# Kernel tuning notes

Hardware: AMD Instinct MI355X
Metric: run time of the kernel (lower is better)

## Reference

```python
import jax, jax.numpy as jnp
import numpy as np

B, L, D_MODEL = 2, 2048, 1024
HEADS, DH, K = 8, 128, 64  # d_head = d_model // heads, kernel_width window
DILATIONS = np.array([1, 1, 2, 2, 4, 4, 8, 8], dtype=np.int32)  # per-head dilation


def setup_inputs() -> dict:
    key = jax.random.key(0)
    ks = jax.random.split(key, 8)
    s_in = 1.0 / np.sqrt(D_MODEL)       # kaiming-uniform-ish fan_in bound
    s_c = 1.0 / np.sqrt(HEADS * DH)
    return {
        "query": jax.random.normal(ks[0], (B, L, D_MODEL), dtype=jnp.float32),
        "key": jax.random.normal(ks[1], (B, L, D_MODEL), dtype=jnp.float32),
        "value": jax.random.normal(ks[2], (B, L, D_MODEL), dtype=jnp.float32),
        "Wq": jax.random.uniform(ks[3], (HEADS, DH, D_MODEL), minval=-s_in, maxval=s_in),
        "bq": jnp.zeros((HEADS, DH), dtype=jnp.float32),
        "Wk": jax.random.uniform(ks[4], (HEADS, DH, D_MODEL), minval=-s_in, maxval=s_in),
        "bk": jnp.zeros((HEADS, DH), dtype=jnp.float32),
        "Wv": jax.random.uniform(ks[5], (HEADS, DH, D_MODEL), minval=-s_in, maxval=s_in),
        "bv": jnp.zeros((HEADS, DH), dtype=jnp.float32),
        "Wc": jax.random.uniform(ks[6], (D_MODEL, HEADS * DH), minval=-s_c, maxval=s_c),
        "bc": jnp.zeros((D_MODEL,), dtype=jnp.float32),
    }


def reference(query, key, value, Wq, bq, Wk, bk, Wv, bv, Wc, bc):
    Lq = query.shape[-2]
    # per-head linear projections: [B,L,D] x [H,DH,D] -> [B,H,L,DH]
    q = jnp.einsum('bld,hed->bhle', query, Wq) + bq[:, None, :]
    k = jnp.einsum('bld,hed->bhle', key, Wk) + bk[:, None, :]
    v = jnp.einsum('bld,hed->bhle', value, Wv) + bv[:, None, :]

    # dilated, centered local windows (per-head dilation)
    offsets = jnp.arange(K) - (K - 1) // 2                     # [K]
    dil = jnp.asarray(DILATIONS)                               # [H]
    idx = (jnp.arange(Lq)[None, :, None]
           + offsets[None, None, :] * dil[:, None, None])      # [H, L, K]
    valid = (idx >= 0) & (idx < Lq)
    idxc = jnp.clip(idx, 0, Lq - 1)

    # gather per-head windows: x [B,H,L,DH], idx [H,L,K] -> [B,H,L,K,DH]
    gather = jax.vmap(lambda xh, ih: xh[:, ih], in_axes=(1, 0), out_axes=1)
    k_win = gather(k, idxc)
    v_win = gather(v, idxc)

    # banded attention (original applies no 1/sqrt(d) scaling)
    scores = jnp.einsum('bhld,bhlkd->bhlk', q, k_win)
    scores = jnp.where(valid[None], scores, jnp.asarray(-1e9, scores.dtype))
    attn = jax.nn.softmax(scores, axis=-1)
    out = jnp.einsum('bhlk,bhlkd->bhld', attn, v_win)

    # merge heads and collapse back to d_model
    out = out.transpose(0, 2, 1, 3).reshape(out.shape[0], Lq, HEADS * DH)
    return out @ Wc.T + bc
```

## Files before the change

### kernel.cpp

```cpp
#include <hip/hip_runtime.h>
#include <hip/hip_bf16.h>
#include <stdint.h>

#define NB 2
#define LQ 2048
#define DMODEL 1024
#define NH 8
#define DH 128
#define KWIN 64

typedef __attribute__((ext_vector_type(8))) short short8;
typedef __attribute__((ext_vector_type(4))) float f32x4;

#define AS1 __attribute__((address_space(1)))
#define AS3 __attribute__((address_space(3)))

__device__ __forceinline__ ushort f2bf(float f) {
  uint u = __float_as_uint(f);
  return (ushort)((u + 0x7fffu + ((u >> 16) & 1u)) >> 16);
}
__device__ __forceinline__ float bflo(uint u) { return __uint_as_float(u << 16); }
__device__ __forceinline__ float bfhi(uint u) { return __uint_as_float(u & 0xffff0000u); }

__global__ void cvt_w(const float4* __restrict__ a, const float4* __restrict__ b,
                      const float4* __restrict__ c, const float4* __restrict__ d,
                      ushort* __restrict__ da, ushort* __restrict__ db,
                      ushort* __restrict__ dc, ushort* __restrict__ dd, int n4) {
  int stride = gridDim.x * blockDim.x;
  for (int i = blockIdx.x * blockDim.x + threadIdx.x; i < n4; i += stride) {
    float4 x = a[i], y = b[i], z = c[i], w = d[i];
    *(ushort4*)(da + 4 * (size_t)i) = make_ushort4(f2bf(x.x), f2bf(x.y), f2bf(x.z), f2bf(x.w));
    *(ushort4*)(db + 4 * (size_t)i) = make_ushort4(f2bf(y.x), f2bf(y.y), f2bf(y.z), f2bf(y.w));
    *(ushort4*)(dc + 4 * (size_t)i) = make_ushort4(f2bf(z.x), f2bf(z.y), f2bf(z.z), f2bf(z.w));
    *(ushort4*)(dd + 4 * (size_t)i) = make_ushort4(f2bf(w.x), f2bf(w.y), f2bf(w.z), f2bf(w.w));
  }
}

__global__ __launch_bounds__(512, 2) void gemm256f(
    const float* __restrict__ A0f, const ushort* __restrict__ B0,
    const float* __restrict__ c0, ushort* __restrict__ D0,
    const float* __restrict__ A1f, const ushort* __restrict__ B1,
    const float* __restrict__ c1, ushort* __restrict__ D1,
    const float* __restrict__ A2f, const ushort* __restrict__ B2,
    const float* __restrict__ c2, ushort* __restrict__ D2,
    int M, int N, int Kd) {
  const int gx = gridDim.x, gy = gridDim.y;
  const int nblk = gx * gy * gridDim.z;
  const int fid = (blockIdx.z * gy + blockIdx.y) * gx + blockIdx.x;
  const int cpx = nblk >> 3;
  const int nid = (fid & 7) * cpx + (fid >> 3);
  const int z = nid / (gx * gy);
  const int rem = nid % (gx * gy);
  const int m0 = (rem / gx) * 256;
  const int n0 = (rem % gx) * 256;

  const float* Af = (z == 0) ? A0f : ((z == 1) ? A1f : A2f);
  const ushort* Bt = (z == 0) ? B0 : ((z == 1) ? B1 : B2);
  const float* bias = (z == 0) ? c0 : ((z == 1) ? c1 : c2);
  ushort* Cv = (z == 0) ? D0 : ((z == 1) ? D1 : D2);

  __shared__ ushort LDS[4][16384];

  const int tid = threadIdx.x;
  const int wave = tid >> 6, lane = tid & 63;
  const int wm = wave >> 2, wn = wave & 3;
  const int lrow = lane & 15, kgrp = lane >> 4;

  const int ac0 = wave * 128 + lane;
  const int ac1 = ac0 + 64;
  const float* gA0 = Af + (size_t)(m0 + (ac0 >> 2)) * Kd + (ac0 & 3) * 8;
  const float* gA1 = Af + (size_t)(m0 + (ac1 >> 2)) * Kd + (ac1 & 3) * 8;

  const int o0 = tid * 16;
  const int o1 = o0 + 8192;
  const ushort* gB0 = Bt + (size_t)(n0 + (o0 >> 6)) * Kd + ((o0 & 63) >> 1);
  const ushort* gB1 = Bt + (size_t)(n0 + (o1 >> 6)) * Kd + ((o1 & 63) >> 1);

  float4 fa0[4], fa1[4];

  auto AISSUE = [&](int tt, float4* d) {
    const float* s0 = gA0 + (tt << 5);
    const float* s1 = gA1 + (tt << 5);
    d[0] = *(const float4*)(s0);
    d[1] = *(const float4*)(s0 + 4);
    d[2] = *(const float4*)(s1);
    d[3] = *(const float4*)(s1 + 4);
  };
  auto BISSUE = [&](int tt) {
    ushort* sl = &LDS[tt & 3][0];
    __builtin_amdgcn_global_load_lds((const AS1 void*)(gB0 + (tt << 5)),
                                     (AS3 void*)(sl + 8192 + (o0 >> 1)), 16, 0, 0);
    __builtin_amdgcn_global_load_lds((const AS1 void*)(gB1 + (tt << 5)),
                                     (AS3 void*)(sl + 8192 + (o1 >> 1)), 16, 0, 0);
  };
  auto AWRITE = [&](int tt, const float4* d) {
    ushort* sl = &LDS[tt & 3][0];
    short8 w0, w1;
    w0[0] = (short)f2bf(d[0].x); w0[1] = (short)f2bf(d[0].y);
    w0[2] = (short)f2bf(d[0].z); w0[3] = (short)f2bf(d[0].w);
    w0[4] = (short)f2bf(d[1].x); w0[5] = (short)f2bf(d[1].y);
    w0[6] = (short)f2bf(d[1].z); w0[7] = (short)f2bf(d[1].w);
    w1[0] = (short)f2bf(d[2].x); w1[1] = (short)f2bf(d[2].y);
    w1[2] = (short)f2bf(d[2].z); w1[3] = (short)f2bf(d[2].w);
    w1[4] = (short)f2bf(d[3].x); w1[5] = (short)f2bf(d[3].y);
    w1[6] = (short)f2bf(d[3].z); w1[7] = (short)f2bf(d[3].w);
    *(short8*)(sl + ac0 * 8) = w0;
    *(short8*)(sl + ac1 * 8) = w1;
  };

  int aoff[8], boff[4];
#pragma unroll
  for (int mi = 0; mi < 8; ++mi) aoff[mi] = (wm * 128 + mi * 16 + lrow) * 32 + kgrp * 8;
#pragma unroll
  for (int ni = 0; ni < 4; ++ni) boff[ni] = 8192 + (wn * 64 + ni * 16 + lrow) * 32 + kgrp * 8;

  f32x4 acc[8][4] = {};
  const int NT = Kd >> 5;

  AISSUE(0, fa0); BISSUE(0);
  AISSUE(1, fa1); BISSUE(1);
  asm volatile("s_waitcnt vmcnt(6)" ::: "memory");
  __builtin_amdgcn_sched_barrier(0);
  AWRITE(0, fa0);
  AISSUE(2, fa0); BISSUE(2);
  asm volatile("s_waitcnt lgkmcnt(0)" ::: "memory");
  __builtin_amdgcn_sched_barrier(0);
  __builtin_amdgcn_s_barrier();

  auto BODY = [&](int t, float4* S) {
    if (t < NT - 1) {
      if (t < NT - 2) {
        asm volatile("s_waitcnt vmcnt(6)" ::: "memory");
      } else {
        asm volatile("s_waitcnt vmcnt(0)" ::: "memory");
      }
      __builtin_amdgcn_sched_barrier(0);
      AWRITE(t + 1, S);
    }
    if (t + 3 < NT) { AISSUE(t + 3, S); BISSUE(t + 3); }

    const ushort* sl = &LDS[t & 3][0];
    short8 af[8], bfr[4];
#pragma unroll
    for (int m = 0; m < 8; ++m) af[m] = *(const short8*)(sl + aoff[m]);
#pragma unroll
    for (int n = 0; n < 4; ++n) bfr[n] = *(const short8*)(sl + boff[n]);
    asm volatile("s_waitcnt lgkmcnt(0)" ::: "memory");
    __builtin_amdgcn_sched_barrier(0);
    __builtin_amdgcn_s_barrier();
    __builtin_amdgcn_sched_barrier(0);

    __builtin_amdgcn_s_setprio(1);
#pragma unroll
    for (int m = 0; m < 8; ++m)
#pragma unroll
      for (int n = 0; n < 4; ++n)
        acc[m][n] = __builtin_amdgcn_mfma_f32_16x16x32_bf16(af[m], bfr[n], acc[m][n], 0, 0, 0);
    __builtin_amdgcn_s_setprio(0);
    __builtin_amdgcn_sched_barrier(0);
  };

  for (int t = 0; t < NT; t += 2) {
    BODY(t, fa1);
    BODY(t + 1, fa0);
  }

  const int cbase = n0 + wn * 64;
  const int rbase = m0 + wm * 128;
  float bv[4];
#pragma unroll
  for (int n = 0; n < 4; ++n) bv[n] = bias[cbase + n * 16 + lrow];

#pragma unroll
  for (int m = 0; m < 8; ++m) {
#pragma unroll
    for (int n = 0; n < 4; ++n) {
      const int col = cbase + n * 16 + lrow;
#pragma unroll
      for (int j = 0; j < 4; ++j) {
        const int row = rbase + m * 16 + kgrp * 4 + j;
        Cv[(size_t)row * N + col] = f2bf(acc[m][n][j] + bv[n]);
      }
    }
  }
}

__global__ __launch_bounds__(256, 4) void gemm_out(
    const ushort* __restrict__ A, const ushort* __restrict__ Bt,
    const float* __restrict__ bias, float* __restrict__ Cv, int M, int N, int Kd) {
  const int gx = gridDim.x, gy = gridDim.y;
  const int nblk = gx * gy;
  const int fid = blockIdx.y * gx + blockIdx.x;
  const int cpx = nblk >> 3;
  const int nid = (fid & 7) * cpx + (fid >> 3);
  const int m0 = (nid / gx) * 128;
  const int n0 = (nid % gx) * 128;

  __shared__ ushort As[2][128 * 32];
  __shared__ ushort Bs[2][128 * 32];

  const int tid = threadIdx.x;
  const int wave = tid >> 6, lane = tid & 63;
  const int wm = wave >> 1, wn = wave & 1;
  const int lrow = lane & 15, kgrp = lane >> 4;

  const int b0 = tid * 16;
  const int b1 = b0 + 4096;
  const int r0 = b0 >> 6, cc0 = (b0 & 63) >> 1;
  const int r1 = b1 >> 6, cc1 = (b1 & 63) >> 1;

  const ushort* gA0 = A + (size_t)(m0 + r0) * Kd + cc0;
  const ushort* gA1 = A + (size_t)(m0 + r1) * Kd + cc1;
  const ushort* gB0 = Bt + (size_t)(n0 + r0) * Kd + cc0;
  const ushort* gB1 = Bt + (size_t)(n0 + r1) * Kd + cc1;

  auto stage = [&](int buf, int kt) {
    __builtin_amdgcn_global_load_lds((const AS1 void*)(gA0 + kt),
                                     (AS3 void*)(As[buf] + (b0 >> 1)), 16, 0, 0);
    __builtin_amdgcn_global_load_lds((const AS1 void*)(gA1 + kt),
                                     (AS3 void*)(As[buf] + (b1 >> 1)), 16, 0, 0);
    __builtin_amdgcn_global_load_lds((const AS1 void*)(gB0 + kt),
                                     (AS3 void*)(Bs[buf] + (b0 >> 1)), 16, 0, 0);
    __builtin_amdgcn_global_load_lds((const AS1 void*)(gB1 + kt),
                                     (AS3 void*)(Bs[buf] + (b1 >> 1)), 16, 0, 0);
  };

  f32x4 acc[4][4] = {};

  auto compute = [&](int buf) {
    short8 af[4], bfr[4];
#pragma unroll
    for (int m = 0; m < 4; ++m)
      af[m] = *(const short8*)(As[buf] + (wm * 64 + m * 16 + lrow) * 32 + kgrp * 8);
#pragma unroll
    for (int n = 0; n < 4; ++n)
      bfr[n] = *(const short8*)(Bs[buf] + (wn * 64 + n * 16 + lrow) * 32 + kgrp * 8);
#pragma unroll
    for (int m = 0; m < 4; ++m)
#pragma unroll
      for (int n = 0; n < 4; ++n)
        acc[m][n] = __builtin_amdgcn_mfma_f32_16x16x32_bf16(af[m], bfr[n], acc[m][n], 0, 0, 0);
  };

  const int nt = Kd >> 5;
  stage(0, 0);
  __syncthreads();
  int cur = 0;
  for (int it = 0; it < nt - 1; ++it) {
    stage(cur ^ 1, (it + 1) << 5);
    compute(cur);
    __syncthreads();
    cur ^= 1;
  }
  compute(cur);

  const int cbase = n0 + wn * 64;
  const int rbase = m0 + wm * 64;
  float bv[4];
#pragma unroll
  for (int n = 0; n < 4; ++n) bv[n] = bias[cbase + n * 16 + lrow];

#pragma unroll
  for (int m = 0; m < 4; ++m) {
#pragma unroll
    for (int n = 0; n < 4; ++n) {
      const int col = cbase + n * 16 + lrow;
#pragma unroll
      for (int j = 0; j < 4; ++j) {
        const int row = rbase + m * 16 + kgrp * 4 + j;
        Cv[(size_t)row * N + col] = acc[m][n][j] + bv[n];
      }
    }
  }
}

__global__ __launch_bounds__(128) void banded_attn_mfma(
    const ushort* __restrict__ qp, const ushort* __restrict__ kp,
    const ushort* __restrict__ vp, ushort* __restrict__ ao) {
  __shared__ ushort Qs[32 * 128];
  __shared__ ushort Ks[96 * 128];
  __shared__ ushort Vs[112 * 128];
  __shared__ ushort Ps[2][16 * 104];
  __shared__ ushort Os[2][16 * 128];

  const int tid = threadIdx.x;
  const int wv = tid >> 6;
  const int lane = tid & 63;
  const int lrow = lane & 15, kgrp = lane >> 4;

  const int blk = blockIdx.x;
  const int chunk = blk & 63;
  const int h = (blk >> 6) & 7;
  const int b = blk >> 9;
  const int sh = h >> 1;
  const int dil = 1 << sh;
  const int Ld = LQ >> sh;
  const int rres = chunk >> (6 - sh);
  const int tile = chunk & ((64 >> sh) - 1);
  const int t0 = tile << 5;
  const int p0 = t0 - 32;

  const size_t headoff = (size_t)h * DH;
  const size_t bbase = (size_t)b * LQ * (NH * DH);

  const int srow = lane >> 4;
  const int sc = lane & 15;
  for (int it = wv; it < 60; it += 2) {
    int rbase, pstart;
    const ushort* g;
    ushort* ld;
    if (it < 8) {
      rbase = it * 4; pstart = t0; g = qp; ld = Qs;
    } else if (it < 32) {
      rbase = (it - 8) * 4; pstart = p0; g = kp; ld = Ks;
    } else {
      rbase = (it - 32) * 4; pstart = p0; g = vp; ld = Vs;
    }
    int row = rbase + srow;
    int key = (row ^ (row >> 3)) & 7;
    int cs = sc ^ key;
    int t = pstart + row;
    t = t < 0 ? 0 : (t >= Ld ? Ld - 1 : t);
    int l = rres + t * dil;
    const ushort* src = g + bbase + (size_t)l * (NH * DH) + headoff + cs * 8;
    __builtin_amdgcn_global_load_lds((const AS1 void*)src,
                                     (AS3 void*)(ld + rbase * 128), 16, 0, 0);
  }
  __syncthreads();

  const int iblk = wv << 4;
  f32x4 accs[5] = {};
#pragma unroll
  for (int ks = 0; ks < 4; ++ks) {
    const int qrow = iblk + lrow;
    const int qslot = (ks * 4 + kgrp) ^ ((qrow ^ (qrow >> 3)) & 7);
    short8 qf = *(const short8*)(Qs + qrow * 128 + qslot * 8);
#pragma unroll
    for (int t = 0; t < 5; ++t) {
      const int krow = (wv + t) * 16 + lrow;
      const int kslot = (ks * 4 + kgrp) ^ ((krow ^ (krow >> 3)) & 7);
      short8 kf = *(const short8*)(Ks + krow * 128 + kslot * 8);
      accs[t] = __builtin_amdgcn_mfma_f32_16x16x32_bf16(qf, kf, accs[t], 0, 0, 0);
    }
  }

  float dens[4];
#pragma unroll
  for (int j = 0; j < 4; ++j) {
    const int i_b = iblk + kgrp * 4 + j;
    float mj = -1e30f;
#pragma unroll
    for (int t = 0; t < 5; ++t) {
      const int jj = (wv + t) * 16 + lrow;
      const int p = p0 + jj;
      const bool ok = (jj >= i_b + 1) && (jj <= i_b + 64) && (p >= 0) && (p < Ld);
      float v = ok ? accs[t][j] : -1e30f;
      accs[t][j] = v;
      mj = fmaxf(mj, v);
    }
#pragma unroll
    for (int off = 1; off < 16; off <<= 1) mj = fmaxf(mj, __shfl_xor(mj, off));
    float dj = 0.f;
#pragma unroll
    for (int t = 0; t < 5; ++t) {
      float e = __expf(accs[t][j] - mj);
      accs[t][j] = e;
      dj += e;
    }
#pragma unroll
    for (int off = 1; off < 16; off <<= 1) dj += __shfl_xor(dj, off);
    dens[j] = dj;
  }

  ushort* Pw = Ps[wv];
#pragma unroll
  for (int j = 0; j < 4; ++j) {
    const int prow = kgrp * 4 + j;
#pragma unroll
    for (int t = 0; t < 5; ++t) Pw[prow * 104 + t * 16 + lrow] = f2bf(accs[t][j]);
    Pw[prow * 104 + 80 + lrow] = 0;
  }

  f32x4 accv[8] = {};
#pragma unroll
  for (int ks = 0; ks < 3; ++ks) {
    short8 pf = *(const short8*)(Pw + lrow * 104 + ks * 32 + kgrp * 8);
#pragma unroll
    for (int dt = 0; dt < 8; ++dt) {
      short8 vf;
#pragma unroll
      for (int rr = 0; rr < 8; ++rr) {
        const int vrow = iblk + ks * 32 + kgrp * 8 + rr;
        const int d = dt * 16 + lrow;
        const int slot = (d >> 3) ^ ((vrow ^ (vrow >> 3)) & 7);
        vf[rr] = (short)Vs[vrow * 128 + slot * 8 + (d & 7)];
      }
      accv[dt] = __builtin_amdgcn_mfma_f32_16x16x32_bf16(pf, vf, accv[dt], 0, 0, 0);
    }
  }

  ushort* Ow = Os[wv];
#pragma unroll
  for (int j = 0; j < 4; ++j) {
    const float inv = 1.f / dens[j];
    const int orow = kgrp * 4 + j;
#pragma unroll
    for (int dt = 0; dt < 8; ++dt)
      Ow[orow * 128 + dt * 16 + lrow] = f2bf(accv[dt][j] * inv);
  }
#pragma unroll
  for (int pass = 0; pass < 4; ++pass) {
    const int i_loc = pass * 4 + srow;
    const int tq = t0 + iblk + i_loc;
    const int l = rres + tq * dil;
    short8 vvv = *(const short8*)(Ow + i_loc * 128 + sc * 8);
    *(short8*)(ao + bbase + (size_t)l * (NH * DH) + headoff + sc * 8) = vvv;
  }
}

extern "C" void kernel_launch(void* const* d_in, const int* in_sizes, int n_in,
                              void* d_out, int out_size, void* d_ws, size_t ws_size,
                              hipStream_t stream) {
  const float* q = (const float*)d_in[0];
  const float* k = (const float*)d_in[1];
  const float* v = (const float*)d_in[2];
  const float* Wq = (const float*)d_in[3];
  const float* bq = (const float*)d_in[4];
  const float* Wk = (const float*)d_in[5];
  const float* bk = (const float*)d_in[6];
  const float* Wv = (const float*)d_in[7];
  const float* bv = (const float*)d_in[8];
  const float* Wc = (const float*)d_in[9];
  const float* bc = (const float*)d_in[10];

  const size_t NIN = (size_t)NB * LQ * DMODEL;
  const size_t NW = (size_t)NH * DH * DMODEL;

  ushort* wqb = (ushort*)d_ws;
  ushort* wkb = wqb + NW;
  ushort* wvb = wkb + NW;
  ushort* wcb = wvb + NW;
  ushort* qp = wcb + NW;
  ushort* kp = qp + NIN;
  ushort* vp = kp + NIN;
  ushort* aob = vp + NIN;

  hipLaunchKernelGGL(cvt_w, dim3(1024), dim3(256), 0, stream,
                     (const float4*)Wq, (const float4*)Wk, (const float4*)Wv,
                     (const float4*)Wc, wqb, wkb, wvb, wcb, (int)(NW / 4));

  dim3 g1(DMODEL / 256, (NB * LQ) / 256, 3);
  hipLaunchKernelGGL(gemm256f, g1, dim3(512), 0, stream,
                     q, wqb, bq, qp,
                     k, wkb, bk, kp,
                     v, wvb, bv, vp,
                     NB * LQ, DMODEL, DMODEL);

  hipLaunchKernelGGL(banded_attn_mfma, dim3(NB * NH * 64), dim3(128), 0, stream,
                     qp, kp, vp, aob);

  dim3 g2(DMODEL / 128, (NB * LQ) / 128);
  hipLaunchKernelGGL(gemm_out, g2, dim3(256), 0, stream,
                     aob, wcb, bc, (float*)d_out, NB * LQ, DMODEL, DMODEL);
}
```

Baseline: 101.4 us.

## Shrink output GEMM tile to 128x64 and reorder QKV GEMM pipeline stage

```diff
diff --git a/kernel.cpp b/kernel.cpp
--- a/kernel.cpp
+++ b/kernel.cpp
@@ -19,8 +19,6 @@
   uint u = __float_as_uint(f);
   return (ushort)((u + 0x7fffu + ((u >> 16) & 1u)) >> 16);
 }
-__device__ __forceinline__ float bflo(uint u) { return __uint_as_float(u << 16); }
-__device__ __forceinline__ float bfhi(uint u) { return __uint_as_float(u & 0xffff0000u); }
 
 __global__ void cvt_w(const float4* __restrict__ a, const float4* __restrict__ b,
                       const float4* __restrict__ c, const float4* __restrict__ d,
@@ -36,7 +34,7 @@
   }
 }
 
-__global__ __launch_bounds__(512, 2) void gemm256f(
+__global__ __launch_bounds__(512, 2) void gemm256r(
     const float* __restrict__ A0f, const ushort* __restrict__ B0,
     const float* __restrict__ c0, ushort* __restrict__ D0,
     const float* __restrict__ A1f, const ushort* __restrict__ B1,
@@ -47,8 +45,7 @@
   const int gx = gridDim.x, gy = gridDim.y;
   const int nblk = gx * gy * gridDim.z;
   const int fid = (blockIdx.z * gy + blockIdx.y) * gx + blockIdx.x;
-  const int cpx = nblk >> 3;
-  const int nid = (fid & 7) * cpx + (fid >> 3);
+  const int nid = (fid & 7) * (nblk >> 3) + (fid >> 3);
   const int z = nid / (gx * gy);
   const int rem = nid % (gx * gy);
   const int m0 = (rem / gx) * 256;
@@ -66,21 +63,17 @@
   const int wm = wave >> 2, wn = wave & 3;
   const int lrow = lane & 15, kgrp = lane >> 4;
 
-  const int ac0 = wave * 128 + lane;
-  const int ac1 = ac0 + 64;
-  const float* gA0 = Af + (size_t)(m0 + (ac0 >> 2)) * Kd + (ac0 & 3) * 8;
-  const float* gA1 = Af + (size_t)(m0 + (ac1 >> 2)) * Kd + (ac1 & 3) * 8;
-
-  const int o0 = tid * 16;
-  const int o1 = o0 + 8192;
+  const float* gAc0 = Af + (size_t)(m0 + (tid >> 2)) * Kd + (tid & 3) * 8;
+  const float* gAc1 = Af + (size_t)(m0 + 128 + (tid >> 2)) * Kd + (tid & 3) * 8;
+  const int o0 = tid * 16, o1 = o0 + 8192;
   const ushort* gB0 = Bt + (size_t)(n0 + (o0 >> 6)) * Kd + ((o0 & 63) >> 1);
   const ushort* gB1 = Bt + (size_t)(n0 + (o1 >> 6)) * Kd + ((o1 & 63) >> 1);
 
   float4 fa0[4], fa1[4];
 
   auto AISSUE = [&](int tt, float4* d) {
-    const float* s0 = gA0 + (tt << 5);
-    const float* s1 = gA1 + (tt << 5);
+    const float* s0 = gAc0 + (tt << 5);
+    const float* s1 = gAc1 + (tt << 5);
     d[0] = *(const float4*)(s0);
     d[1] = *(const float4*)(s0 + 4);
     d[2] = *(const float4*)(s1);
@@ -89,9 +82,9 @@
   auto BISSUE = [&](int tt) {
     ushort* sl = &LDS[tt & 3][0];
     __builtin_amdgcn_global_load_lds((const AS1 void*)(gB0 + (tt << 5)),
-                                     (AS3 void*)(sl + 8192 + (o0 >> 1)), 16, 0, 0);
+                                     (AS3 void*)(sl + 8192 + tid * 8), 16, 0, 0);
     __builtin_amdgcn_global_load_lds((const AS1 void*)(gB1 + (tt << 5)),
-                                     (AS3 void*)(sl + 8192 + (o1 >> 1)), 16, 0, 0);
+                                     (AS3 void*)(sl + 8192 + 4096 + tid * 8), 16, 0, 0);
   };
   auto AWRITE = [&](int tt, const float4* d) {
     ushort* sl = &LDS[tt & 3][0];
@@ -104,8 +97,8 @@
     w1[2] = (short)f2bf(d[2].z); w1[3] = (short)f2bf(d[2].w);
     w1[4] = (short)f2bf(d[3].x); w1[5] = (short)f2bf(d[3].y);
     w1[6] = (short)f2bf(d[3].z); w1[7] = (short)f2bf(d[3].w);
-    *(short8*)(sl + ac0 * 8) = w0;
-    *(short8*)(sl + ac1 * 8) = w1;
+    *(short8*)(sl + tid * 8) = w0;
+    *(short8*)(sl + 4096 + tid * 8) = w1;
   };
 
   int aoff[8], boff[4];
@@ -127,24 +120,23 @@
   __builtin_amdgcn_sched_barrier(0);
   __builtin_amdgcn_s_barrier();
 
-  auto BODY = [&](int t, float4* S) {
-    if (t < NT - 1) {
-      if (t < NT - 2) {
-        asm volatile("s_waitcnt vmcnt(6)" ::: "memory");
-      } else {
-        asm volatile("s_waitcnt vmcnt(0)" ::: "memory");
-      }
-      __builtin_amdgcn_sched_barrier(0);
-      AWRITE(t + 1, S);
-    }
-    if (t + 3 < NT) { AISSUE(t + 3, S); BISSUE(t + 3); }
-
+  auto BODY = [&](int t, float4* Swr) {
     const ushort* sl = &LDS[t & 3][0];
     short8 af[8], bfr[4];
 #pragma unroll
     for (int m = 0; m < 8; ++m) af[m] = *(const short8*)(sl + aoff[m]);
 #pragma unroll
     for (int n = 0; n < 4; ++n) bfr[n] = *(const short8*)(sl + boff[n]);
+
+    if (t + 2 < NT) {
+      asm volatile("s_waitcnt vmcnt(6)" ::: "memory");
+    } else {
+      asm volatile("s_waitcnt vmcnt(0)" ::: "memory");
+    }
+    __builtin_amdgcn_sched_barrier(0);
+    if (t + 1 < NT) AWRITE(t + 1, Swr);
+    if (t + 3 < NT) { AISSUE(t + 3, Swr); BISSUE(t + 3); }
+
     asm volatile("s_waitcnt lgkmcnt(0)" ::: "memory");
     __builtin_amdgcn_sched_barrier(0);
     __builtin_amdgcn_s_barrier();
@@ -170,76 +162,62 @@
   float bv[4];
 #pragma unroll
   for (int n = 0; n < 4; ++n) bv[n] = bias[cbase + n * 16 + lrow];
-
-#pragma unroll
-  for (int m = 0; m < 8; ++m) {
+#pragma unroll
+  for (int m = 0; m < 8; ++m)
 #pragma unroll
     for (int n = 0; n < 4; ++n) {
       const int col = cbase + n * 16 + lrow;
 #pragma unroll
-      for (int j = 0; j < 4; ++j) {
-        const int row = rbase + m * 16 + kgrp * 4 + j;
-        Cv[(size_t)row * N + col] = f2bf(acc[m][n][j] + bv[n]);
-      }
-    }
-  }
-}
-
-__global__ __launch_bounds__(256, 4) void gemm_out(
+      for (int j = 0; j < 4; ++j)
+        Cv[(size_t)(rbase + m * 16 + kgrp * 4 + j) * N + col] = f2bf(acc[m][n][j] + bv[n]);
+    }
+}
+
+__global__ __launch_bounds__(256, 4) void gemm_out2(
     const ushort* __restrict__ A, const ushort* __restrict__ Bt,
     const float* __restrict__ bias, float* __restrict__ Cv, int M, int N, int Kd) {
-  const int gx = gridDim.x, gy = gridDim.y;
-  const int nblk = gx * gy;
+  const int gx = gridDim.x;
+  const int nblk = gx * gridDim.y;
   const int fid = blockIdx.y * gx + blockIdx.x;
-  const int cpx = nblk >> 3;
-  const int nid = (fid & 7) * cpx + (fid >> 3);
+  const int nid = (fid & 7) * (nblk >> 3) + (fid >> 3);
   const int m0 = (nid / gx) * 128;
-  const int n0 = (nid % gx) * 128;
+  const int n0 = (nid % gx) * 64;
 
   __shared__ ushort As[2][128 * 32];
-  __shared__ ushort Bs[2][128 * 32];
+  __shared__ ushort Bs[2][64 * 32];
 
   const int tid = threadIdx.x;
   const int wave = tid >> 6, lane = tid & 63;
-  const int wm = wave >> 1, wn = wave & 1;
+  const int wmO = wave >> 1, wnO = wave & 1;
   const int lrow = lane & 15, kgrp = lane >> 4;
 
-  const int b0 = tid * 16;
-  const int b1 = b0 + 4096;
-  const int r0 = b0 >> 6, cc0 = (b0 & 63) >> 1;
-  const int r1 = b1 >> 6, cc1 = (b1 & 63) >> 1;
-
-  const ushort* gA0 = A + (size_t)(m0 + r0) * Kd + cc0;
-  const ushort* gA1 = A + (size_t)(m0 + r1) * Kd + cc1;
-  const ushort* gB0 = Bt + (size_t)(n0 + r0) * Kd + cc0;
-  const ushort* gB1 = Bt + (size_t)(n0 + r1) * Kd + cc1;
+  const ushort* gA0 = A + (size_t)(m0 + (tid >> 2)) * Kd + (tid & 3) * 8;
+  const ushort* gA1 = A + (size_t)(m0 + 64 + (tid >> 2)) * Kd + (tid & 3) * 8;
+  const ushort* gB = Bt + (size_t)(n0 + (tid >> 2)) * Kd + (tid & 3) * 8;
 
   auto stage = [&](int buf, int kt) {
     __builtin_amdgcn_global_load_lds((const AS1 void*)(gA0 + kt),
-                                     (AS3 void*)(As[buf] + (b0 >> 1)), 16, 0, 0);
+                                     (AS3 void*)(As[buf] + tid * 8), 16, 0, 0);
     __builtin_amdgcn_global_load_lds((const AS1 void*)(gA1 + kt),
-                                     (AS3 void*)(As[buf] + (b1 >> 1)), 16, 0, 0);
-    __builtin_amdgcn_global_load_lds((const AS1 void*)(gB0 + kt),
-                                     (AS3 void*)(Bs[buf] + (b0 >> 1)), 16, 0, 0);
-    __builtin_amdgcn_global_load_lds((const AS1 void*)(gB1 + kt),
-                                     (AS3 void*)(Bs[buf] + (b1 >> 1)), 16, 0, 0);
-  };
-
-  f32x4 acc[4][4] = {};
-
+                                     (AS3 void*)(As[buf] + 2048 + tid * 8), 16, 0, 0);
+    __builtin_amdgcn_global_load_lds((const AS1 void*)(gB + kt),
+                                     (AS3 void*)(Bs[buf] + tid * 8), 16, 0, 0);
+  };
+
+  f32x4 acc[4][2] = {};
   auto compute = [&](int buf) {
-    short8 af[4], bfr[4];
-#pragma unroll
-    for (int m = 0; m < 4; ++m)
-      af[m] = *(const short8*)(As[buf] + (wm * 64 + m * 16 + lrow) * 32 + kgrp * 8);
-#pragma unroll
-    for (int n = 0; n < 4; ++n)
-      bfr[n] = *(const short8*)(Bs[buf] + (wn * 64 + n * 16 + lrow) * 32 + kgrp * 8);
-#pragma unroll
-    for (int m = 0; m < 4; ++m)
-#pragma unroll
-      for (int n = 0; n < 4; ++n)
-        acc[m][n] = __builtin_amdgcn_mfma_f32_16x16x32_bf16(af[m], bfr[n], acc[m][n], 0, 0, 0);
+    short8 af[4], bfr[2];
+#pragma unroll
+    for (int mi = 0; mi < 4; ++mi)
+      af[mi] = *(const short8*)(As[buf] + (wmO * 64 + mi * 16 + lrow) * 32 + kgrp * 8);
+#pragma unroll
+    for (int ni = 0; ni < 2; ++ni)
+      bfr[ni] = *(const short8*)(Bs[buf] + (wnO * 32 + ni * 16 + lrow) * 32 + kgrp * 8);
+#pragma unroll
+    for (int mi = 0; mi < 4; ++mi)
+#pragma unroll
+      for (int ni = 0; ni < 2; ++ni)
+        acc[mi][ni] = __builtin_amdgcn_mfma_f32_16x16x32_bf16(af[mi], bfr[ni], acc[mi][ni], 0, 0, 0);
   };
 
   const int nt = Kd >> 5;
@@ -254,24 +232,20 @@
   }
   compute(cur);
 
-  const int cbase = n0 + wn * 64;
-  const int rbase = m0 + wm * 64;
-  float bv[4];
-#pragma unroll
-  for (int n = 0; n < 4; ++n) bv[n] = bias[cbase + n * 16 + lrow];
-
-#pragma unroll
-  for (int m = 0; m < 4; ++m) {
-#pragma unroll
-    for (int n = 0; n < 4; ++n) {
-      const int col = cbase + n * 16 + lrow;
-#pragma unroll
-      for (int j = 0; j < 4; ++j) {
-        const int row = rbase + m * 16 + kgrp * 4 + j;
-        Cv[(size_t)row * N + col] = acc[m][n][j] + bv[n];
-      }
-    }
-  }
+  const int cbase = n0 + wnO * 32;
+  const int rbase = m0 + wmO * 64;
+  float bv[2];
+#pragma unroll
+  for (int ni = 0; ni < 2; ++ni) bv[ni] = bias[cbase + ni * 16 + lrow];
+#pragma unroll
+  for (int mi = 0; mi < 4; ++mi)
+#pragma unroll
+    for (int ni = 0; ni < 2; ++ni) {
+      const int col = cbase + ni * 16 + lrow;
+#pragma unroll
+      for (int j = 0; j < 4; ++j)
+        Cv[(size_t)(rbase + mi * 16 + kgrp * 4 + j) * N + col] = acc[mi][ni][j] + bv[ni];
+    }
 }
 
 __global__ __launch_bounds__(128) void banded_attn_mfma(
@@ -450,7 +424,7 @@
                      (const float4*)Wc, wqb, wkb, wvb, wcb, (int)(NW / 4));
 
   dim3 g1(DMODEL / 256, (NB * LQ) / 256, 3);
-  hipLaunchKernelGGL(gemm256f, g1, dim3(512), 0, stream,
+  hipLaunchKernelGGL(gemm256r, g1, dim3(512), 0, stream,
                      q, wqb, bq, qp,
                      k, wkb, bk, kp,
                      v, wvb, bv, vp,
@@ -459,7 +433,7 @@
   hipLaunchKernelGGL(banded_attn_mfma, dim3(NB * NH * 64), dim3(128), 0, stream,
                      qp, kp, vp, aob);
 
-  dim3 g2(DMODEL / 128, (NB * LQ) / 128);
-  hipLaunchKernelGGL(gemm_out, g2, dim3(256), 0, stream,
+  dim3 g2(DMODEL / 64, (NB * LQ) / 128);
+  hipLaunchKernelGGL(gemm_out2, g2, dim3(256), 0, stream,
                      aob, wcb, bc, (float*)d_out, NB * LQ, DMODEL, DMODEL);
 }
```

Result: faster. 97.35 us (-4.0%).
